# Kernel tuning notes

Measured on AMD Instinct MI355X. Metric: run time of the kernel, lower is better.

## Reference

```python
import jax, jax.numpy as jnp
import numpy as np

N_NODES = 100000
N_EDGES = 1600000
N_GRAPHS = 256
IN_F = 64   # global_features (GNN input dim)
OUT_F = 64  # node_features (GNN output dim)


def setup_inputs() -> dict:
    key = jax.random.key(0)
    ks = jax.random.split(key, 8)
    x = jax.random.normal(ks[0], (N_NODES, IN_F), dtype=jnp.float32)
    edge_index = jax.random.randint(ks[1], (2, N_EDGES), 0, N_NODES, dtype=jnp.int64)
    batch = jnp.sort(jax.random.randint(ks[2], (N_NODES,), 0, N_GRAPHS, dtype=jnp.int64))
    # GNNLayer linear: in=global_features, out=node_features
    W_gnn = jax.random.normal(ks[3], (IN_F, OUT_F), dtype=jnp.float32) / np.sqrt(IN_F)
    b_gnn = jnp.zeros((OUT_F,), dtype=jnp.float32)
    # global_attention: Linear(node_features, 1)
    W_att = jax.random.normal(ks[4], (OUT_F, 1), dtype=jnp.float32) / np.sqrt(OUT_F)
    b_att = jnp.zeros((1,), dtype=jnp.float32)
    return {"x": x, "edge_index": edge_index, "batch": batch,
            "W_gnn": W_gnn, "b_gnn": b_gnn, "W_att": W_att, "b_att": b_att}


def reference(x, edge_index, batch, W_gnn, b_gnn, W_att, b_att):
    src, dst = edge_index[0], edge_index[1]
    # --- GNN message passing layer: aggregate neighbor features, transform ---
    agg = jax.ops.segment_sum(x[src], dst, num_segments=N_NODES)  # [N, IN_F]
    h = jax.nn.relu((x + agg) @ W_gnn + b_gnn)                    # [N, OUT_F]
    # --- attention scores + scatter softmax over batch segments ---
    scores = (h @ W_att + b_att)[:, 0]                            # [N]
    seg_max = jax.ops.segment_max(scores, batch, num_segments=N_GRAPHS)
    e = jnp.exp(scores - seg_max[batch])
    denom = jax.ops.segment_sum(e, batch, num_segments=N_GRAPHS)
    w = e / denom[batch]                                          # [N]
    # --- weighted scatter-add pooling ---
    out = jax.ops.segment_sum(w[:, None] * h, batch, num_segments=N_GRAPHS)
    return out  # [N_GRAPHS, OUT_F]
```

## Files before the change

### kernel.cpp

```cpp
#include <hip/hip_runtime.h>

#define N_NODES  100000
#define N_EDGES  1600000
#define N_GRAPHS 256
#define F        64


#define GRID_PRE 1024
#define BLK      256

#define NBUCK    196
#define BCAP     9216
#define BSTRIDE  16
#define EPB      1563
#define REPT     7

#define CAST_ELEMS (N_NODES * F / 4)
#define NT_BLOCKS  ((N_NODES + 63) / 64)

typedef short  bf16x8 __attribute__((ext_vector_type(8)));
typedef float  f32x4  __attribute__((ext_vector_type(4)));

__device__ __forceinline__ unsigned short f2bf(float f) {
    unsigned int u = __float_as_uint(f);
    u += 0x7FFFu + ((u >> 16) & 1u);
    return (unsigned short)(u >> 16);
}
__device__ __forceinline__ float bfu(unsigned short u) {
    return __uint_as_float((unsigned)u << 16);
}

__global__ __launch_bounds__(BLK) void bin_kernel(
        const int* __restrict__ src, const int* __restrict__ dst,
        unsigned int* __restrict__ pairs, int* __restrict__ balloc) {
    __shared__ int hist[NBUCK], roffs[NBUCK], bbase[NBUCK], curs[NBUCK];
    __shared__ int wsum[8];
    __shared__ unsigned int   stage[EPB];
    __shared__ unsigned short bstage[EPB];
    int tid = threadIdx.x, bid = blockIdx.x;
    int lane = tid & 63, wv = tid >> 6;
    int base = bid * EPB;
    int m = min(EPB, N_EDGES - base);

    for (int k = tid; k < NBUCK; k += BLK) hist[k] = 0;
    __syncthreads();

    int de[REPT], se[REPT];
    #pragma unroll
    for (int r = 0; r < REPT; ++r) {
        int e = tid + r * BLK;
        if (e < m) {
            de[r] = dst[base + e];
            se[r] = src[base + e];
            atomicAdd(&hist[de[r] >> 9], 1);
        } else { de[r] = -1; se[r] = 0; }
    }
    __syncthreads();

    int cnt = (tid < NBUCK) ? hist[tid] : 0;
    int v = cnt;
    #pragma unroll
    for (int o = 1; o < 64; o <<= 1) { int u = __shfl_up(v, o, 64); if (lane >= o) v += u; }
    if (lane == 63) wsum[wv] = v;
    __syncthreads();
    if (tid < 4) {
        int sv = wsum[tid];
        int u = __shfl_up(sv, 1, 64); if (tid >= 1) sv += u;
        u     = __shfl_up(sv, 2, 64); if (tid >= 2) sv += u;
        wsum[tid] = sv;
    }
    __syncthreads();
    if (wv > 0) v += wsum[wv - 1];
    if (tid < NBUCK) {
        int excl = v - cnt;
        roffs[tid] = excl;
        curs[tid]  = excl;
        bbase[tid] = tid * BCAP + atomicAdd(&balloc[tid * BSTRIDE], cnt);
    }
    __syncthreads();

    #pragma unroll
    for (int r = 0; r < REPT; ++r) {
        if (de[r] >= 0) {
            int bk  = de[r] >> 9;
            int pos = atomicAdd(&curs[bk], 1);
            stage[pos]  = ((unsigned)(de[r] & 511) << 17) | (unsigned)se[r];
            bstage[pos] = (unsigned short)bk;
        }
    }
    __syncthreads();
    for (int e = tid; e < m; e += BLK) {
        int bk = bstage[e];
        pairs[bbase[bk] + (e - roffs[bk])] = stage[e];
    }
}

__global__ __launch_bounds__(BLK) void sortcast_kernel(
        const float* __restrict__ x, unsigned short* __restrict__ xh,
        const unsigned int* __restrict__ pairs, int* __restrict__ eidx,
        int* __restrict__ nbeg, int* __restrict__ nend,
        const int* __restrict__ balloc,
        float* __restrict__ out, float* __restrict__ denom) {
    __shared__ int hist[512], curs[512], wsum[8];
    int tid = threadIdx.x, bid = blockIdx.x;
    int lane = tid & 63, wv = tid >> 6;

    if (bid < NBUCK) {
        int E     = balloc[bid * BSTRIDE];
        int base  = bid * BCAP;
        int node0 = bid << 9;
        int nn    = min(512, N_NODES - node0);

        hist[tid] = 0; hist[tid + 256] = 0;
        __syncthreads();
        for (int i = tid; i < E; i += BLK)
            atomicAdd(&hist[pairs[base + i] >> 17], 1);
        __syncthreads();

        int c0 = hist[tid];
        int v0 = c0;
        #pragma unroll
        for (int o = 1; o < 64; o <<= 1) { int u = __shfl_up(v0, o, 64); if (lane >= o) v0 += u; }
        if (lane == 63) wsum[wv] = v0;
        __syncthreads();
        if (tid < 4) {
            int sv = wsum[tid];
            int u = __shfl_up(sv, 1, 64); if (tid >= 1) sv += u;
            u     = __shfl_up(sv, 2, 64); if (tid >= 2) sv += u;
            wsum[tid] = sv;
        }
        __syncthreads();
        if (wv > 0) v0 += wsum[wv - 1];
        int total0 = wsum[3];

        int c1 = hist[tid + 256];
        int v1 = c1;
        #pragma unroll
        for (int o = 1; o < 64; o <<= 1) { int u = __shfl_up(v1, o, 64); if (lane >= o) v1 += u; }
        if (lane == 63) wsum[4 + wv] = v1;
        __syncthreads();
        if (tid < 4) {
            int sv = wsum[4 + tid];
            int u = __shfl_up(sv, 1, 64); if (tid >= 1) sv += u;
            u     = __shfl_up(sv, 2, 64); if (tid >= 2) sv += u;
            wsum[4 + tid] = sv;
        }
        __syncthreads();
        if (wv > 0) v1 += wsum[4 + wv - 1];
        v1 += total0;

        int e0 = v0 - c0, e1 = v1 - c1;
        curs[tid] = e0; curs[tid + 256] = e1;
        if (tid < nn)       { nbeg[node0 + tid] = base + e0;
                              nend[node0 + tid] = base + e0 + c0; }
        if (tid + 256 < nn) { nbeg[node0 + tid + 256] = base + e1;
                              nend[node0 + tid + 256] = base + e1 + c1; }
        __syncthreads();

        for (int i = tid; i < E; i += BLK) {
            unsigned int p = pairs[base + i];
            int pos = atomicAdd(&curs[p >> 17], 1);
            eidx[base + pos] = (int)(p & 0x1FFFFu);
        }
    } else {
        if (bid == NBUCK) {
            for (int i = tid; i < N_GRAPHS * F; i += BLK) out[i] = 0.f;
            denom[tid] = 0.f;
        }
        int i0      = (bid - NBUCK) * BLK + tid;
        int cstride = (GRID_PRE - NBUCK) * BLK;
        for (int i = i0; i < CAST_ELEMS; i += cstride) {
            float4 v4 = ((const float4*)x)[i];
            ushort4 o;
            o.x = f2bf(v4.x); o.y = f2bf(v4.y); o.z = f2bf(v4.z); o.w = f2bf(v4.w);
            ((ushort4*)xh)[i] = o;
        }
    }
}

__global__ __launch_bounds__(BLK) void gather_mfma_kernel(
        const unsigned short* __restrict__ xh,
        const int*   __restrict__ nbeg,
        const int*   __restrict__ nend,
        const int*   __restrict__ eidx,
        const int*   __restrict__ batch,
        const float* __restrict__ Wg,
        const float* __restrict__ bg,
        const float* __restrict__ Wa,
        const float* __restrict__ ba,
        float*       __restrict__ out,
        float*       __restrict__ denom) {
    __shared__ unsigned short shAhi[64 * 64];
    __shared__ unsigned short shAlo[64 * 64];
    __shared__ unsigned short shW[64 * 64];

    int tid  = threadIdx.x;
    int bid  = blockIdx.x;
    int lane = tid & 63;
    int w    = tid >> 6;

    for (int i = tid; i < 64 * 64; i += BLK) {
        int k = i >> 6, n = i & 63;
        shW[n * 64 + k] = f2bf(Wg[i]);
    }
    __syncthreads();

    int tile_base = bid * 64 + w * 16;
    if (tile_base >= N_NODES) return;

    int nb = 0, ne = 0;
    {
        int nd = tile_base + lane;
        if (lane < 16 && nd < N_NODES) { nb = nbeg[nd]; ne = nend[nd]; }
    }
    int pb_c = __builtin_amdgcn_readlane(nb, 0);
    int pe_c = __builtin_amdgcn_readlane(ne, 0);
    int sl_c = (pb_c + lane < pe_c) ? eidx[pb_c + lane] : 0;

    for (int q = 0; q < 16; ++q) {
        int node = tile_base + q;
        int pb = pb_c, pe = pe_c, sl = sl_c;
        if (q + 1 < 16) {
            pb_c = __builtin_amdgcn_readlane(nb, q + 1);
            pe_c = __builtin_amdgcn_readlane(ne, q + 1);
            sl_c = (pb_c + lane < pe_c) ? eidx[pb_c + lane] : 0;
        }
        float y = 0.f;
        if (node < N_NODES) {
            y = bfu(xh[node * 64 + lane]);
            int c0 = min(pe - pb, 64);
            int e = 0;
            for (; e + 8 <= c0; e += 8) {
                int i0 = __builtin_amdgcn_readlane(sl, e + 0);
                int i1 = __builtin_amdgcn_readlane(sl, e + 1);
                int i2 = __builtin_amdgcn_readlane(sl, e + 2);
                int i3 = __builtin_amdgcn_readlane(sl, e + 3);
                int i4 = __builtin_amdgcn_readlane(sl, e + 4);
                int i5 = __builtin_amdgcn_readlane(sl, e + 5);
                int i6 = __builtin_amdgcn_readlane(sl, e + 6);
                int i7 = __builtin_amdgcn_readlane(sl, e + 7);
                float v0 = bfu(xh[i0 * 64 + lane]);
                float v1 = bfu(xh[i1 * 64 + lane]);
                float v2 = bfu(xh[i2 * 64 + lane]);
                float v3 = bfu(xh[i3 * 64 + lane]);
                float v4 = bfu(xh[i4 * 64 + lane]);
                float v5 = bfu(xh[i5 * 64 + lane]);
                float v6 = bfu(xh[i6 * 64 + lane]);
                float v7 = bfu(xh[i7 * 64 + lane]);
                y += ((v0 + v1) + (v2 + v3)) + ((v4 + v5) + (v6 + v7));
            }
            for (; e < c0; ++e) {
                int i0 = __builtin_amdgcn_readlane(sl, e);
                y += bfu(xh[i0 * 64 + lane]);
            }
            for (int b2 = pb + 64; b2 < pe; b2 += 64) {
                int sl2 = (b2 + lane < pe) ? eidx[b2 + lane] : 0;
                int c2 = min(pe - b2, 64);
                int e2 = 0;
                for (; e2 + 8 <= c2; e2 += 8) {
                    int i0 = __builtin_amdgcn_readlane(sl2, e2 + 0);
                    int i1 = __builtin_amdgcn_readlane(sl2, e2 + 1);
                    int i2 = __builtin_amdgcn_readlane(sl2, e2 + 2);
                    int i3 = __builtin_amdgcn_readlane(sl2, e2 + 3);
                    int i4 = __builtin_amdgcn_readlane(sl2, e2 + 4);
                    int i5 = __builtin_amdgcn_readlane(sl2, e2 + 5);
                    int i6 = __builtin_amdgcn_readlane(sl2, e2 + 6);
                    int i7 = __builtin_amdgcn_readlane(sl2, e2 + 7);
                    float v0 = bfu(xh[i0 * 64 + lane]);
                    float v1 = bfu(xh[i1 * 64 + lane]);
                    float v2 = bfu(xh[i2 * 64 + lane]);
                    float v3 = bfu(xh[i3 * 64 + lane]);
                    float v4 = bfu(xh[i4 * 64 + lane]);
                    float v5 = bfu(xh[i5 * 64 + lane]);
                    float v6 = bfu(xh[i6 * 64 + lane]);
                    float v7 = bfu(xh[i7 * 64 + lane]);
                    y += ((v0 + v1) + (v2 + v3)) + ((v4 + v5) + (v6 + v7));
                }
                for (; e2 < c2; ++e2) {
                    int i0 = __builtin_amdgcn_readlane(sl2, e2);
                    y += bfu(xh[i0 * 64 + lane]);
                }
            }
        }
        unsigned short hh = f2bf(y);
        float lo = y - bfu(hh);
        unsigned short hl = f2bf(lo);
        shAhi[(w * 16 + q) * 64 + lane] = hh;
        shAlo[(w * 16 + q) * 64 + lane] = hl;
    }

    int lr = lane & 15, lq = lane >> 4;
    const bf16x8 ah0 = *(const bf16x8*)&shAhi[(w * 16 + lr) * 64 +  0 + 8 * lq];
    const bf16x8 ah1 = *(const bf16x8*)&shAhi[(w * 16 + lr) * 64 + 32 + 8 * lq];
    const bf16x8 al0 = *(const bf16x8*)&shAlo[(w * 16 + lr) * 64 +  0 + 8 * lq];
    const bf16x8 al1 = *(const bf16x8*)&shAlo[(w * 16 + lr) * 64 + 32 + 8 * lq];

    f32x4 acc0 = {0.f,0.f,0.f,0.f}, acc1 = {0.f,0.f,0.f,0.f};
    f32x4 acc2 = {0.f,0.f,0.f,0.f}, acc3 = {0.f,0.f,0.f,0.f};
    #define DO_TILE(t, accv) { \
        bf16x8 b0 = *(const bf16x8*)&shW[(16*(t) + lr) * 64 +  0 + 8 * lq]; \
        bf16x8 b1 = *(const bf16x8*)&shW[(16*(t) + lr) * 64 + 32 + 8 * lq]; \
        accv = __builtin_amdgcn_mfma_f32_16x16x32_bf16(ah0, b0, accv, 0, 0, 0); \
        accv = __builtin_amdgcn_mfma_f32_16x16x32_bf16(al0, b0, accv, 0, 0, 0); \
        accv = __builtin_amdgcn_mfma_f32_16x16x32_bf16(ah1, b1, accv, 0, 0, 0); \
        accv = __builtin_amdgcn_mfma_f32_16x16x32_bf16(al1, b1, accv, 0, 0, 0); }
    DO_TILE(0, acc0) DO_TILE(1, acc1) DO_TILE(2, acc2) DO_TILE(3, acc3)
    #undef DO_TILE

    float bg0 = bg[lr], bg1 = bg[16 + lr], bg2 = bg[32 + lr], bg3 = bg[48 + lr];
    float wa0 = Wa[lr], wa1 = Wa[16 + lr], wa2 = Wa[32 + lr], wa3 = Wa[48 + lr];
    float ba0 = ba[0];

    float hv0[4], hv1[4], hv2[4], hv3[4];
    #pragma unroll
    for (int r = 0; r < 4; ++r) {
        hv0[r] = fmaxf(acc0[r] + bg0, 0.f);
        hv1[r] = fmaxf(acc1[r] + bg1, 0.f);
        hv2[r] = fmaxf(acc2[r] + bg2, 0.f);
        hv3[r] = fmaxf(acc3[r] + bg3, 0.f);
    }
    float part[4];
    #pragma unroll
    for (int r = 0; r < 4; ++r)
        part[r] = hv0[r] * wa0 + hv1[r] * wa1 + hv2[r] * wa2 + hv3[r] * wa3;
    #pragma unroll
    for (int o = 1; o <= 8; o <<= 1) {
        #pragma unroll
        for (int r = 0; r < 4; ++r) part[r] += __shfl_xor(part[r], o, 64);
    }
    float ev[4]; int gidx[4];
    #pragma unroll
    for (int r = 0; r < 4; ++r) {
        int node = tile_base + 4 * lq + r;
        bool ok = node < N_NODES;
        ev[r]   = ok ? __expf(part[r] + ba0) : 0.f;
        gidx[r] = ok ? batch[node] : 0;
    }
    int gmin = batch[tile_base];
    int glast = tile_base + 15; if (glast >= N_NODES) glast = N_NODES - 1;
    int gmax = batch[glast];

    for (int gg = gmin; gg <= gmax; ++gg) {
        float w0 = (gidx[0] == gg) ? ev[0] : 0.f;
        float w1 = (gidx[1] == gg) ? ev[1] : 0.f;
        float w2 = (gidx[2] == gg) ? ev[2] : 0.f;
        float w3 = (gidx[3] == gg) ? ev[3] : 0.f;
        float p0 = w0 * hv0[0] + w1 * hv0[1] + w2 * hv0[2] + w3 * hv0[3];
        float p1 = w0 * hv1[0] + w1 * hv1[1] + w2 * hv1[2] + w3 * hv1[3];
        float p2 = w0 * hv2[0] + w1 * hv2[1] + w2 * hv2[2] + w3 * hv2[3];
        float p3 = w0 * hv3[0] + w1 * hv3[1] + w2 * hv3[2] + w3 * hv3[3];
        float dn = w0 + w1 + w2 + w3;
        #pragma unroll
        for (int o = 16; o <= 32; o <<= 1) {
            p0 += __shfl_xor(p0, o, 64); p1 += __shfl_xor(p1, o, 64);
            p2 += __shfl_xor(p2, o, 64); p3 += __shfl_xor(p3, o, 64);
            dn += __shfl_xor(dn, o, 64);
        }
        if (lq == 0) {
            atomicAdd(&out[gg * F +  0 + lr], p0);
            atomicAdd(&out[gg * F + 16 + lr], p1);
            atomicAdd(&out[gg * F + 32 + lr], p2);
            atomicAdd(&out[gg * F + 48 + lr], p3);
            if (lr == 0) atomicAdd(&denom[gg], dn);
        }
    }
}

__global__ __launch_bounds__(BLK) void fin_kernel(
        float* __restrict__ out, const float* __restrict__ denom) {
    int i = blockIdx.x * BLK + threadIdx.x;
    if (i >= N_GRAPHS * F) return;
    float d = denom[i >> 6];
    out[i] = (d > 0.f) ? out[i] / d : 0.f;
}

extern "C" void kernel_launch(void* const* d_in, const int* in_sizes, int n_in,
                              void* d_out, int out_size, void* d_ws, size_t ws_size,
                              hipStream_t stream) {
    const float* x     = (const float*)d_in[0];
    const int*   ei    = (const int*)d_in[1];
    const int*   batch = (const int*)d_in[2];
    const float* Wg    = (const float*)d_in[3];
    const float* bg    = (const float*)d_in[4];
    const float* Wa    = (const float*)d_in[5];
    const float* ba    = (const float*)d_in[6];
    float* out = (float*)d_out;

    const int* src = ei;
    const int* dst = ei + N_EDGES;

    char* ws = (char*)d_ws;
    unsigned short* xh     = (unsigned short*)(ws);
    unsigned int*   pairs  = (unsigned int*)(ws + 12800000);
    int*            eidx   = (int*)(ws + 20025344);
    int*            nbeg   = (int*)(ws + 27250688);
    int*            nend   = (int*)(ws + 27652096);
    int*            balloc = (int*)(ws + 28053504);
    float*          denom  = (float*)(ws + 28066048);

    hipMemsetAsync(balloc, 0, NBUCK * BSTRIDE * sizeof(int), stream);
    bin_kernel      <<<GRID_PRE, BLK, 0, stream>>>(src, dst, pairs, balloc);
    sortcast_kernel <<<GRID_PRE, BLK, 0, stream>>>(x, xh, pairs, eidx,
                                                   nbeg, nend, balloc, out, denom);
    gather_mfma_kernel<<<NT_BLOCKS, BLK, 0, stream>>>(xh, nbeg, nend, eidx, batch,
                                                      Wg, bg, Wa, ba, out, denom);
    fin_kernel      <<<64, BLK, 0, stream>>>(out, denom);
}
```

Baseline: 222.0 us.

## Gather neighbor rows with 8-byte loads across lane groups, pad LDS stride

The gather loop now has each wavefront fetch four neighbor rows at once. Sixteen lanes each load 8 bytes (four bf16 features) per row, and the partial sums are reduced with xor shuffles. This replaces one 2-byte load per lane per neighbor, so there are fewer, wider memory transactions. The LDS tiles are padded to a stride of 72 to cut bank conflicts in the MFMA operand reads. The sort kernel moves to 512-thread blocks so each thread scans one histogram bin instead of two. The risk is that the ragged tail iterations waste lanes and the extra shuffle reduction adds instructions.

```diff
diff --git a/kernel.cpp b/kernel.cpp
--- a/kernel.cpp
+++ b/kernel.cpp
@@ -8,6 +8,7 @@
 
 #define GRID_PRE 1024
 #define BLK      256
+#define SBLK     512
 
 #define NBUCK    196
 #define BCAP     9216
@@ -17,6 +18,8 @@
 
 #define CAST_ELEMS (N_NODES * F / 4)
 #define NT_BLOCKS  ((N_NODES + 63) / 64)
+
+#define AST 72
 
 typedef short  bf16x8 __attribute__((ext_vector_type(8)));
 typedef float  f32x4  __attribute__((ext_vector_type(4)));
@@ -95,7 +98,7 @@
     }
 }
 
-__global__ __launch_bounds__(BLK) void sortcast_kernel(
+__global__ __launch_bounds__(SBLK) void sortcast_kernel(
         const float* __restrict__ x, unsigned short* __restrict__ xh,
         const unsigned int* __restrict__ pairs, int* __restrict__ eidx,
         int* __restrict__ nbeg, int* __restrict__ nend,
@@ -111,64 +114,48 @@
         int node0 = bid << 9;
         int nn    = min(512, N_NODES - node0);
 
-        hist[tid] = 0; hist[tid + 256] = 0;
-        __syncthreads();
-        for (int i = tid; i < E; i += BLK)
+        hist[tid] = 0;
+        __syncthreads();
+        for (int i = tid; i < E; i += SBLK)
             atomicAdd(&hist[pairs[base + i] >> 17], 1);
         __syncthreads();
 
-        int c0 = hist[tid];
-        int v0 = c0;
+        int c = hist[tid];
+        int v = c;
         #pragma unroll
-        for (int o = 1; o < 64; o <<= 1) { int u = __shfl_up(v0, o, 64); if (lane >= o) v0 += u; }
-        if (lane == 63) wsum[wv] = v0;
-        __syncthreads();
-        if (tid < 4) {
+        for (int o = 1; o < 64; o <<= 1) { int u = __shfl_up(v, o, 64); if (lane >= o) v += u; }
+        if (lane == 63) wsum[wv] = v;
+        __syncthreads();
+        if (tid < 8) {
             int sv = wsum[tid];
             int u = __shfl_up(sv, 1, 64); if (tid >= 1) sv += u;
             u     = __shfl_up(sv, 2, 64); if (tid >= 2) sv += u;
+            u     = __shfl_up(sv, 4, 64); if (tid >= 4) sv += u;
             wsum[tid] = sv;
         }
         __syncthreads();
-        if (wv > 0) v0 += wsum[wv - 1];
-        int total0 = wsum[3];
-
-        int c1 = hist[tid + 256];
-        int v1 = c1;
-        #pragma unroll
-        for (int o = 1; o < 64; o <<= 1) { int u = __shfl_up(v1, o, 64); if (lane >= o) v1 += u; }
-        if (lane == 63) wsum[4 + wv] = v1;
-        __syncthreads();
-        if (tid < 4) {
-            int sv = wsum[4 + tid];
-            int u = __shfl_up(sv, 1, 64); if (tid >= 1) sv += u;
-            u     = __shfl_up(sv, 2, 64); if (tid >= 2) sv += u;
-            wsum[4 + tid] = sv;
-        }
-        __syncthreads();
-        if (wv > 0) v1 += wsum[4 + wv - 1];
-        v1 += total0;
-
-        int e0 = v0 - c0, e1 = v1 - c1;
-        curs[tid] = e0; curs[tid + 256] = e1;
-        if (tid < nn)       { nbeg[node0 + tid] = base + e0;
-                              nend[node0 + tid] = base + e0 + c0; }
-        if (tid + 256 < nn) { nbeg[node0 + tid + 256] = base + e1;
-                              nend[node0 + tid + 256] = base + e1 + c1; }
-        __syncthreads();
-
-        for (int i = tid; i < E; i += BLK) {
+        if (wv > 0) v += wsum[wv - 1];
+
+        int excl = v - c;
+        curs[tid] = excl;
+        if (tid < nn) {
+            nbeg[node0 + tid] = base + excl;
+            nend[node0 + tid] = base + excl + c;
+        }
+        __syncthreads();
+
+        for (int i = tid; i < E; i += SBLK) {
             unsigned int p = pairs[base + i];
             int pos = atomicAdd(&curs[p >> 17], 1);
             eidx[base + pos] = (int)(p & 0x1FFFFu);
         }
     } else {
         if (bid == NBUCK) {
-            for (int i = tid; i < N_GRAPHS * F; i += BLK) out[i] = 0.f;
-            denom[tid] = 0.f;
-        }
-        int i0      = (bid - NBUCK) * BLK + tid;
-        int cstride = (GRID_PRE - NBUCK) * BLK;
+            for (int i = tid; i < N_GRAPHS * F; i += SBLK) out[i] = 0.f;
+            if (tid < N_GRAPHS) denom[tid] = 0.f;
+        }
+        int i0      = (bid - NBUCK) * SBLK + tid;
+        int cstride = (GRID_PRE - NBUCK) * SBLK;
         for (int i = i0; i < CAST_ELEMS; i += cstride) {
             float4 v4 = ((const float4*)x)[i];
             ushort4 o;
@@ -190,9 +177,9 @@
         const float* __restrict__ ba,
         float*       __restrict__ out,
         float*       __restrict__ denom) {
-    __shared__ unsigned short shAhi[64 * 64];
-    __shared__ unsigned short shAlo[64 * 64];
-    __shared__ unsigned short shW[64 * 64];
+    __shared__ unsigned short shAhi[64 * AST];
+    __shared__ unsigned short shAlo[64 * AST];
+    __shared__ unsigned short shW[64 * AST];
 
     int tid  = threadIdx.x;
     int bid  = blockIdx.x;
@@ -201,12 +188,17 @@
 
     for (int i = tid; i < 64 * 64; i += BLK) {
         int k = i >> 6, n = i & 63;
-        shW[n * 64 + k] = f2bf(Wg[i]);
+        shW[n * AST + k] = f2bf(Wg[i]);
     }
     __syncthreads();
 
     int tile_base = bid * 64 + w * 16;
     if (tile_base >= N_NODES) return;
+
+    int li = lane & 15;
+    int lg = lane >> 4;
+
+    const uint2* xh2 = (const uint2*)xh;
 
     int nb = 0, ne = 0;
     {
@@ -225,81 +217,70 @@
             pe_c = __builtin_amdgcn_readlane(ne, q + 1);
             sl_c = (pb_c + lane < pe_c) ? eidx[pb_c + lane] : 0;
         }
-        float y = 0.f;
+        float y0 = 0.f, y1 = 0.f, y2 = 0.f, y3 = 0.f;
         if (node < N_NODES) {
-            y = bfu(xh[node * 64 + lane]);
+            {
+                uint2 v = xh2[node * 16 + li];
+                if (lg == 0) {
+                    y0 += __uint_as_float(v.x << 16);
+                    y1 += __uint_as_float(v.x & 0xFFFF0000u);
+                    y2 += __uint_as_float(v.y << 16);
+                    y3 += __uint_as_float(v.y & 0xFFFF0000u);
+                }
+            }
             int c0 = min(pe - pb, 64);
-            int e = 0;
-            for (; e + 8 <= c0; e += 8) {
-                int i0 = __builtin_amdgcn_readlane(sl, e + 0);
-                int i1 = __builtin_amdgcn_readlane(sl, e + 1);
-                int i2 = __builtin_amdgcn_readlane(sl, e + 2);
-                int i3 = __builtin_amdgcn_readlane(sl, e + 3);
-                int i4 = __builtin_amdgcn_readlane(sl, e + 4);
-                int i5 = __builtin_amdgcn_readlane(sl, e + 5);
-                int i6 = __builtin_amdgcn_readlane(sl, e + 6);
-                int i7 = __builtin_amdgcn_readlane(sl, e + 7);
-                float v0 = bfu(xh[i0 * 64 + lane]);
-                float v1 = bfu(xh[i1 * 64 + lane]);
-                float v2 = bfu(xh[i2 * 64 + lane]);
-                float v3 = bfu(xh[i3 * 64 + lane]);
-                float v4 = bfu(xh[i4 * 64 + lane]);
-                float v5 = bfu(xh[i5 * 64 + lane]);
-                float v6 = bfu(xh[i6 * 64 + lane]);
-                float v7 = bfu(xh[i7 * 64 + lane]);
-                y += ((v0 + v1) + (v2 + v3)) + ((v4 + v5) + (v6 + v7));
-            }
-            for (; e < c0; ++e) {
-                int i0 = __builtin_amdgcn_readlane(sl, e);
-                y += bfu(xh[i0 * 64 + lane]);
+            for (int e = 0; e < c0; e += 4) {
+                int slot = e + lg;
+                int idx  = __shfl(sl, slot, 64);
+                uint2 v  = xh2[idx * 16 + li];
+                if (slot < c0) {
+                    y0 += __uint_as_float(v.x << 16);
+                    y1 += __uint_as_float(v.x & 0xFFFF0000u);
+                    y2 += __uint_as_float(v.y << 16);
+                    y3 += __uint_as_float(v.y & 0xFFFF0000u);
+                }
             }
             for (int b2 = pb + 64; b2 < pe; b2 += 64) {
                 int sl2 = (b2 + lane < pe) ? eidx[b2 + lane] : 0;
                 int c2 = min(pe - b2, 64);
-                int e2 = 0;
-                for (; e2 + 8 <= c2; e2 += 8) {
-                    int i0 = __builtin_amdgcn_readlane(sl2, e2 + 0);
-                    int i1 = __builtin_amdgcn_readlane(sl2, e2 + 1);
-                    int i2 = __builtin_amdgcn_readlane(sl2, e2 + 2);
-                    int i3 = __builtin_amdgcn_readlane(sl2, e2 + 3);
-                    int i4 = __builtin_amdgcn_readlane(sl2, e2 + 4);
-                    int i5 = __builtin_amdgcn_readlane(sl2, e2 + 5);
-                    int i6 = __builtin_amdgcn_readlane(sl2, e2 + 6);
-                    int i7 = __builtin_amdgcn_readlane(sl2, e2 + 7);
-                    float v0 = bfu(xh[i0 * 64 + lane]);
-                    float v1 = bfu(xh[i1 * 64 + lane]);
-                    float v2 = bfu(xh[i2 * 64 + lane]);
-                    float v3 = bfu(xh[i3 * 64 + lane]);
-                    float v4 = bfu(xh[i4 * 64 + lane]);
-                    float v5 = bfu(xh[i5 * 64 + lane]);
-                    float v6 = bfu(xh[i6 * 64 + lane]);
-                    float v7 = bfu(xh[i7 * 64 + lane]);
-                    y += ((v0 + v1) + (v2 + v3)) + ((v4 + v5) + (v6 + v7));
-                }
-                for (; e2 < c2; ++e2) {
-                    int i0 = __builtin_amdgcn_readlane(sl2, e2);
-                    y += bfu(xh[i0 * 64 + lane]);
+                for (int e = 0; e < c2; e += 4) {
+                    int slot = e + lg;
+                    int idx  = __shfl(sl2, slot, 64);
+                    uint2 v  = xh2[idx * 16 + li];
+                    if (slot < c2) {
+                        y0 += __uint_as_float(v.x << 16);
+                        y1 += __uint_as_float(v.x & 0xFFFF0000u);
+                        y2 += __uint_as_float(v.y << 16);
+                        y3 += __uint_as_float(v.y & 0xFFFF0000u);
+                    }
                 }
             }
         }
-        unsigned short hh = f2bf(y);
-        float lo = y - bfu(hh);
-        unsigned short hl = f2bf(lo);
-        shAhi[(w * 16 + q) * 64 + lane] = hh;
-        shAlo[(w * 16 + q) * 64 + lane] = hl;
+        y0 += __shfl_xor(y0, 16, 64); y0 += __shfl_xor(y0, 32, 64);
+        y1 += __shfl_xor(y1, 16, 64); y1 += __shfl_xor(y1, 32, 64);
+        y2 += __shfl_xor(y2, 16, 64); y2 += __shfl_xor(y2, 32, 64);
+        y3 += __shfl_xor(y3, 16, 64); y3 += __shfl_xor(y3, 32, 64);
+
+        ushort4 ph, pl;
+        ph.x = f2bf(y0); ph.y = f2bf(y1); ph.z = f2bf(y2); ph.w = f2bf(y3);
+        pl.x = f2bf(y0 - bfu(ph.x)); pl.y = f2bf(y1 - bfu(ph.y));
+        pl.z = f2bf(y2 - bfu(ph.z)); pl.w = f2bf(y3 - bfu(ph.w));
+        int row = w * 16 + q;
+        if (lg == 0)      *(ushort4*)&shAhi[row * AST + 4 * li] = ph;
+        else if (lg == 1) *(ushort4*)&shAlo[row * AST + 4 * li] = pl;
     }
 
     int lr = lane & 15, lq = lane >> 4;
-    const bf16x8 ah0 = *(const bf16x8*)&shAhi[(w * 16 + lr) * 64 +  0 + 8 * lq];
-    const bf16x8 ah1 = *(const bf16x8*)&shAhi[(w * 16 + lr) * 64 + 32 + 8 * lq];
-    const bf16x8 al0 = *(const bf16x8*)&shAlo[(w * 16 + lr) * 64 +  0 + 8 * lq];
-    const bf16x8 al1 = *(const bf16x8*)&shAlo[(w * 16 + lr) * 64 + 32 + 8 * lq];
+    const bf16x8 ah0 = *(const bf16x8*)&shAhi[(w * 16 + lr) * AST +  0 + 8 * lq];
+    const bf16x8 ah1 = *(const bf16x8*)&shAhi[(w * 16 + lr) * AST + 32 + 8 * lq];
+    const bf16x8 al0 = *(const bf16x8*)&shAlo[(w * 16 + lr) * AST +  0 + 8 * lq];
+    const bf16x8 al1 = *(const bf16x8*)&shAlo[(w * 16 + lr) * AST + 32 + 8 * lq];
 
     f32x4 acc0 = {0.f,0.f,0.f,0.f}, acc1 = {0.f,0.f,0.f,0.f};
     f32x4 acc2 = {0.f,0.f,0.f,0.f}, acc3 = {0.f,0.f,0.f,0.f};
     #define DO_TILE(t, accv) { \
-        bf16x8 b0 = *(const bf16x8*)&shW[(16*(t) + lr) * 64 +  0 + 8 * lq]; \
-        bf16x8 b1 = *(const bf16x8*)&shW[(16*(t) + lr) * 64 + 32 + 8 * lq]; \
+        bf16x8 b0 = *(const bf16x8*)&shW[(16*(t) + lr) * AST +  0 + 8 * lq]; \
+        bf16x8 b1 = *(const bf16x8*)&shW[(16*(t) + lr) * AST + 32 + 8 * lq]; \
         accv = __builtin_amdgcn_mfma_f32_16x16x32_bf16(ah0, b0, accv, 0, 0, 0); \
         accv = __builtin_amdgcn_mfma_f32_16x16x32_bf16(al0, b0, accv, 0, 0, 0); \
         accv = __builtin_amdgcn_mfma_f32_16x16x32_bf16(ah1, b1, accv, 0, 0, 0); \
@@ -399,10 +380,10 @@
     float*          denom  = (float*)(ws + 28066048);
 
     hipMemsetAsync(balloc, 0, NBUCK * BSTRIDE * sizeof(int), stream);
-    bin_kernel      <<<GRID_PRE, BLK, 0, stream>>>(src, dst, pairs, balloc);
-    sortcast_kernel <<<GRID_PRE, BLK, 0, stream>>>(x, xh, pairs, eidx,
-                                                   nbeg, nend, balloc, out, denom);
+    bin_kernel        <<<GRID_PRE, BLK, 0, stream>>>(src, dst, pairs, balloc);
+    sortcast_kernel   <<<GRID_PRE, SBLK, 0, stream>>>(x, xh, pairs, eidx,
+                                                      nbeg, nend, balloc, out, denom);
     gather_mfma_kernel<<<NT_BLOCKS, BLK, 0, stream>>>(xh, nbeg, nend, eidx, batch,
                                                       Wg, bg, Wa, ba, out, denom);
-    fin_kernel      <<<64, BLK, 0, stream>>>(out, denom);
-}
+    fin_kernel        <<<64, BLK, 0, stream>>>(out, denom);
+}
```

Result: no change. 219.9 us (-0.9%).
